# Kernel tuning notes

Hardware: AMD Instinct MI355X
Metric: run time of the kernel (lower is better)

Reference implementation:

```python
import jax, jax.numpy as jnp
import numpy as np
import math

# LLaMA-7B-style int8 attention (torch-int Int8LlamaAttention)
B, S, HID, NH, HD = 2, 1024, 4096, 32, 128
THETA = 10000.0
# per-tensor quantization scales (as produced by from_float)
S_IN, S_W, S_B = 0.02, 0.01, 0.1
S_Q, S_K, S_V, S_O = 0.05, 0.05, 0.05, 0.05


def _rope_tables(position_ids):
    inv_freq = 1.0 / (THETA ** (jnp.arange(0, HD, 2, dtype=jnp.float32) / HD))
    freqs = position_ids.astype(jnp.float32)[..., None] * inv_freq  # [B,S,HD//2]
    emb = jnp.concatenate([freqs, freqs], axis=-1)  # [B,S,HD]
    return jnp.cos(emb)[:, None], jnp.sin(emb)[:, None]  # [B,1,S,HD]


def _rotate_half(x):
    return jnp.concatenate([-x[..., HD // 2:], x[..., :HD // 2]], axis=-1)


def _quant_i8(x):
    return jnp.clip(jnp.round(x), -128, 127).astype(jnp.int8)


def _w8a8b8o8(x_i8, w_i8, b_i8, alpha, beta):
    # int8 GEMM with int32 accumulation, fused dequant-requant to int8
    acc = jnp.einsum('bsk,nk->bsn', x_i8.astype(jnp.int32), w_i8.astype(jnp.int32))
    return _quant_i8(acc.astype(jnp.float32) * alpha + b_i8.astype(jnp.float32) * beta)


def setup_inputs() -> dict:
    key = jax.random.key(0)
    ks = jax.random.split(key, 9)
    ri8 = lambda k, shp: jax.random.randint(k, shp, -127, 128, dtype=jnp.int8)
    return {
        'hidden_states': jax.random.normal(ks[0], (B, S, HID), jnp.float32),
        'position_ids': jnp.broadcast_to(jnp.arange(S, dtype=jnp.int32), (B, S)),
        'w_q': ri8(ks[1], (HID, HID)),
        'w_k': ri8(ks[2], (HID, HID)),
        'w_v': ri8(ks[3], (HID, HID)),
        'w_o': ri8(ks[4], (HID, HID)),
        'b_q': ri8(ks[5], (HID,)),
        'b_k': ri8(ks[6], (HID,)),
        'b_v': ri8(ks[7], (HID,)),
        'b_o': jax.random.normal(ks[8], (HID,), jnp.float32) * 0.01,
    }


def reference(hidden_states, position_ids, w_q, w_k, w_v, w_o, b_q, b_k, b_v, b_o):
    # quantize activations, run int8 q/k/v projections (W8A8B8O8Linear)
    x_i8 = _quant_i8(hidden_states / S_IN)
    q = _w8a8b8o8(x_i8, w_q, b_q, S_IN * S_W / S_Q, S_B / S_Q)
    k = _w8a8b8o8(x_i8, w_k, b_k, S_IN * S_W / S_K, S_B / S_K)
    v = _w8a8b8o8(x_i8, w_v, b_v, S_IN * S_W / S_V, S_B / S_V)
    to_heads = lambda t: t.reshape(B, S, NH, HD).transpose(0, 2, 1, 3)  # [B,NH,S,HD]
    q, k, v = to_heads(q), to_heads(k), to_heads(v)
    # RoPE applied on dequantized int8 values, requantized for the int8 qk bmm
    cos, sin = _rope_tables(position_ids)
    qf, kf = q.astype(jnp.float32), k.astype(jnp.float32)
    q_i8 = _quant_i8(qf * cos + _rotate_half(qf) * sin)
    k_i8 = _quant_i8(kf * cos + _rotate_half(kf) * sin)
    # BMM_S8T_S8N_F32T: int8 QK^T -> fp32 with scale s_q*s_k, then /sqrt(d)
    attn = jnp.einsum('bhsd,bhtd->bhst', q_i8.astype(jnp.int32), k_i8.astype(jnp.int32))
    attn = attn.astype(jnp.float32) * (S_Q * S_K) / math.sqrt(HD)
    # NOTE: source never applies the attention mask (`attn_weights = attn_weights`)
    p = jax.nn.softmax(attn, axis=-1)
    # probs quantized to int8 with scale 1/127 for BMM_S8T_S8N_S8T
    p_i8 = _quant_i8(p * 127.0)
    ctx = jnp.einsum('bhst,bhtd->bhsd', p_i8.astype(jnp.int32), v.astype(jnp.int32))
    ctx_i8 = _quant_i8(ctx.astype(jnp.float32) * ((1.0 / 127.0) * S_V / S_O))
    ctx_i8 = ctx_i8.transpose(0, 2, 1, 3).reshape(B, S, HID)
    # W8A8BFP32OFP32 o_proj: int8 GEMM, fp32 output + fp32 bias
    out = jnp.einsum('bsk,nk->bsn', ctx_i8.astype(jnp.int32), w_o.astype(jnp.int32))
    return out.astype(jnp.float32) * (S_O * S_W) + b_o
```

## Files before the change

### kernel.cpp

```cpp
#include <hip/hip_runtime.h>
#include <hip/hip_bf16.h>
#include <cstdint>
#include <cstddef>

typedef int v4i __attribute__((ext_vector_type(4)));

#define NH 32
#define HD 128
#define SEQ 1024
#define HID 4096
#define BB 2
#define BKB 128

__device__ __forceinline__ signed char quant_i8(float x) {
    float r = rintf(x);
    r = fminf(fmaxf(r, -128.0f), 127.0f);
    return (signed char)r;
}

#define GLOAD_LDS16(g, l) \
    __builtin_amdgcn_global_load_lds((const __attribute__((address_space(1))) void*)(g), \
                                     (__attribute__((address_space(3))) void*)(l), 16, 0, 0)

__global__ __launch_bounds__(256) void pack4_i8_kernel(
    const int* __restrict__ s0, const int* __restrict__ s1,
    const int* __restrict__ s2, const int* __restrict__ s3,
    signed char* __restrict__ d0, signed char* __restrict__ d1,
    signed char* __restrict__ d2, signed char* __restrict__ d3, int n4)
{
    int i = blockIdx.x * 256 + threadIdx.x;
    int which = i / n4;
    int idx = i - which * n4;
    const int* src = (which == 0) ? s0 : (which == 1) ? s1 : (which == 2) ? s2 : s3;
    signed char* dst = (which == 0) ? d0 : (which == 1) ? d1 : (which == 2) ? d2 : d3;
    int4 v = ((const int4*)src)[idx];
    char4 c;
    c.x = (signed char)v.x; c.y = (signed char)v.y;
    c.z = (signed char)v.z; c.w = (signed char)v.w;
    ((char4*)dst)[idx] = c;
}

__global__ __launch_bounds__(256) void quant_x_kernel(const float* __restrict__ src,
                                                      signed char* __restrict__ dst, int n4) {
    int i = blockIdx.x * 256 + threadIdx.x;
    if (i >= n4) return;
    float4 v = ((const float4*)src)[i];
    char4 c;
    c.x = quant_i8(v.x * 50.0f);
    c.y = quant_i8(v.y * 50.0f);
    c.z = quant_i8(v.z * 50.0f);
    c.w = quant_i8(v.w * 50.0f);
    ((char4*)dst)[i] = c;
}

template<bool F32OUT>
__global__ __launch_bounds__(256) void gemm_i8_lds(
    const signed char* __restrict__ A, const signed char* __restrict__ Bw,
    const void* __restrict__ bias, void* __restrict__ outp,
    int M, int N, int K, float alpha, float beta)
{
    __shared__ __align__(16) signed char sA[128 * BKB];
    __shared__ __align__(16) signed char sB[128 * BKB];

    const int t    = threadIdx.x;
    const int w    = t >> 6;
    const int lane = t & 63;
    const int m0   = blockIdx.y * 128;
    const int n0   = blockIdx.x * 128;
    const int lm   = lane & 15;
    const int quad = lane >> 4;
    const int wm   = (w >> 1) * 64;
    const int wn   = (w & 1) * 64;

    int srow[4], skc[4];
    #pragma unroll
    for (int p = 0; p < 4; p++) {
        int si = t + 256 * p;
        int row = si >> 3;
        srow[p] = row;
        skc[p] = ((si & 7) - (row >> 1)) & 7;
    }

    v4i acc[4][4] = {};

    for (int k0 = 0; k0 < K; k0 += BKB) {
        __syncthreads();
        #pragma unroll
        for (int p = 0; p < 4; p++) {
            const signed char* ga = A + (size_t)(m0 + srow[p]) * K + k0 + skc[p] * 16;
            GLOAD_LDS16(ga, sA + t * 16 + p * 4096);
        }
        #pragma unroll
        for (int p = 0; p < 4; p++) {
            const signed char* gb = Bw + (size_t)(n0 + srow[p]) * K + k0 + skc[p] * 16;
            GLOAD_LDS16(gb, sB + t * 16 + p * 4096);
        }
        __syncthreads();

        #pragma unroll
        for (int ks = 0; ks < 2; ks++) {
            v4i af[4], bf[4];
            #pragma unroll
            for (int i = 0; i < 4; i++) {
                int row = wm + 16 * i + lm;
                int slot = (ks * 4 + quad + (lm >> 1)) & 7;
                af[i] = *(const v4i*)(sA + row * BKB + slot * 16);
            }
            #pragma unroll
            for (int j = 0; j < 4; j++) {
                int row = wn + 16 * j + lm;
                int slot = (ks * 4 + quad + (lm >> 1)) & 7;
                bf[j] = *(const v4i*)(sB + row * BKB + slot * 16);
            }
            #pragma unroll
            for (int i = 0; i < 4; i++)
                #pragma unroll
                for (int j = 0; j < 4; j++)
                    acc[i][j] = __builtin_amdgcn_mfma_i32_16x16x64_i8(af[i], bf[j], acc[i][j], 0, 0, 0);
        }
    }

    const int orow = quad * 4;
    #pragma unroll
    for (int i = 0; i < 4; i++) {
        #pragma unroll
        for (int j = 0; j < 4; j++) {
            #pragma unroll
            for (int r = 0; r < 4; r++) {
                int row = m0 + wm + 16 * i + orow + r;
                int col = n0 + wn + 16 * j + lm;
                float v = (float)acc[i][j][r];
                if (F32OUT) {
                    ((float*)outp)[(size_t)row * N + col] = v * alpha + ((const float*)bias)[col];
                } else {
                    float q = v * alpha + (float)((const int*)bias)[col] * beta;
                    ((signed char*)outp)[(size_t)row * N + col] = quant_i8(q);
                }
            }
        }
    }
}

__global__ __launch_bounds__(128) void rope_kernel(
    const int* __restrict__ pos_ids, signed char* __restrict__ q,
    signed char* __restrict__ k, const signed char* __restrict__ v,
    signed char* __restrict__ vt)
{
    int bid = blockIdx.x;
    int h = bid & (NH - 1);
    int s = (bid >> 5) & (SEQ - 1);
    int b = bid >> 15;
    int d = threadIdx.x;
    size_t base = ((size_t)(b * SEQ + s) * NH + h) * (size_t)HD;
    int pos = pos_ids[b * SEQ + s];

    float inv = expf(-(float)(2 * (d & 63)) * (9.210340371976184f / 128.0f));
    float freq = (float)pos * inv;
    float cs = cosf(freq), sn = sinf(freq);

    float qd = (float)q[base + d];
    float qp = (float)q[base + (d ^ 64)];
    float kd = (float)k[base + d];
    float kp = (float)k[base + (d ^ 64)];
    signed char vd = v[base + d];
    __syncthreads();

    float rotq = (d < 64) ? -qp : qp;
    float rotk = (d < 64) ? -kp : kp;
    q[base + d] = quant_i8(qd * cs + rotq * sn);
    k[base + d] = quant_i8(kd * cs + rotk * sn);
    vt[((size_t)((b * NH + h) * HD + d)) * SEQ + s] = vd;
}

__global__ __launch_bounds__(256) void attn_kernel(
    const signed char* __restrict__ q, const signed char* __restrict__ k,
    const signed char* __restrict__ vt, signed char* __restrict__ ctx)
{
    __shared__ __align__(16) char smem[65536];
    float* sc = (float*)smem;
    signed char* p8 = (signed char*)smem;

    const int w    = threadIdx.x >> 6;
    const int lane = threadIdx.x & 63;
    const int bid  = blockIdx.x;
    const int mt   = bid & 63;
    const int bh   = bid >> 6;
    const int b    = bh >> 5, h = bh & 31;
    const int m0   = mt * 16;
    const int lm   = lane & 15;
    const int lkb  = (lane >> 4) * 16;
    const int quad = lane >> 4;

    const float SCALE = 0.0025f / 11.313708498984761f;
    const float LOG2E = 1.4426950408889634f;

    const signed char* qbase = q + ((size_t)(b * SEQ + m0 + lm) * NH + h) * (size_t)HD + lkb;
    v4i a0 = *(const v4i*)qbase;
    v4i a1 = *(const v4i*)(qbase + 64);

    #pragma unroll
    for (int j = 0; j < 16; j++) {
        int col = w * 256 + j * 16;
        const signed char* kb = k + ((size_t)(b * SEQ + col + lm) * NH + h) * (size_t)HD + lkb;
        v4i b0 = *(const v4i*)kb;
        v4i b1 = *(const v4i*)(kb + 64);
        v4i acc = {};
        acc = __builtin_amdgcn_mfma_i32_16x16x64_i8(a0, b0, acc, 0, 0, 0);
        acc = __builtin_amdgcn_mfma_i32_16x16x64_i8(a1, b1, acc, 0, 0, 0);
        #pragma unroll
        for (int r = 0; r < 4; r++) {
            int row = quad * 4 + r;
            sc[row * 1024 + col + lm] = (float)acc[r] * SCALE;
        }
    }
    __syncthreads();

    int packed[4][4];
    #pragma unroll
    for (int r = 0; r < 4; r++) {
        int row = w * 4 + r;
        float vals[16];
        #pragma unroll
        for (int c = 0; c < 4; c++) {
            float4 f = *(const float4*)(sc + row * 1024 + c * 256 + lane * 4);
            vals[c * 4 + 0] = f.x; vals[c * 4 + 1] = f.y;
            vals[c * 4 + 2] = f.z; vals[c * 4 + 3] = f.w;
        }
        float mx = -1e30f;
        #pragma unroll
        for (int t = 0; t < 16; t++) mx = fmaxf(mx, vals[t]);
        #pragma unroll
        for (int off = 32; off >= 1; off >>= 1) mx = fmaxf(mx, __shfl_xor(mx, off));
        float sum = 0.f;
        #pragma unroll
        for (int t = 0; t < 16; t++) { vals[t] = exp2f((vals[t] - mx) * LOG2E); sum += vals[t]; }
        #pragma unroll
        for (int off = 32; off >= 1; off >>= 1) sum += __shfl_xor(sum, off);
        float sf = 127.0f / sum;
        #pragma unroll
        for (int c = 0; c < 4; c++) {
            union { signed char cc[4]; int ii; } u;
            #pragma unroll
            for (int t = 0; t < 4; t++) u.cc[t] = quant_i8(vals[c * 4 + t] * sf);
            packed[r][c] = u.ii;
        }
    }
    __syncthreads();

    #pragma unroll
    for (int r = 0; r < 4; r++)
        #pragma unroll
        for (int c = 0; c < 4; c++)
            *(int*)(p8 + (w * 4 + r) * 1040 + c * 256 + lane * 4) = packed[r][c];
    __syncthreads();

    v4i accp[2] = {};
    for (int kk = 0; kk < SEQ; kk += 64) {
        v4i af = *(const v4i*)(p8 + lm * 1040 + kk + lkb);
        #pragma unroll
        for (int j = 0; j < 2; j++) {
            int col = w * 32 + j * 16;
            const signed char* vb = vt + ((size_t)(bh * HD + col + lm)) * (size_t)SEQ + kk + lkb;
            accp[j] = __builtin_amdgcn_mfma_i32_16x16x64_i8(af, *(const v4i*)vb, accp[j], 0, 0, 0);
        }
    }
    #pragma unroll
    for (int j = 0; j < 2; j++) {
        #pragma unroll
        for (int r = 0; r < 4; r++) {
            int row = quad * 4 + r;
            int col = w * 32 + j * 16 + lm;
            ctx[((size_t)(b * SEQ + m0 + row) * NH + h) * (size_t)HD + col] =
                quant_i8((float)accp[j][r] * (1.0f / 127.0f));
        }
    }
}

extern "C" void kernel_launch(void* const* d_in, const int* in_sizes, int n_in,
                              void* d_out, int out_size, void* d_ws, size_t ws_size,
                              hipStream_t stream)
{
    const float* hidden = (const float*)d_in[0];
    const int* pos_ids  = (const int*)d_in[1];
    const int* w_q = (const int*)d_in[2];
    const int* w_k = (const int*)d_in[3];
    const int* w_v = (const int*)d_in[4];
    const int* w_o = (const int*)d_in[5];
    const int* b_q = (const int*)d_in[6];
    const int* b_k = (const int*)d_in[7];
    const int* b_v = (const int*)d_in[8];
    const float* b_o = (const float*)d_in[9];
    float* out = (float*)d_out;

    char* ws = (char*)d_ws;
    const size_t WSZ = (size_t)HID * HID;
    signed char* wq8 = (signed char*)ws;
    signed char* wk8 = wq8 + WSZ;
    signed char* wv8 = wk8 + WSZ;
    signed char* wo8 = wv8 + WSZ;
    signed char* x8  = wo8 + WSZ;
    const size_t ASZ = (size_t)BB * SEQ * HID;
    signed char* q8  = x8 + ASZ;
    signed char* k8  = q8 + ASZ;
    signed char* v8  = k8 + ASZ;
    signed char* vt8 = v8 + ASZ;
    signed char* c8  = vt8 + ASZ;

    int wn4 = HID * HID / 4;
    pack4_i8_kernel<<<4 * wn4 / 256, 256, 0, stream>>>(w_q, w_k, w_v, w_o,
                                                       wq8, wk8, wv8, wo8, wn4);
    int xn4 = (int)(ASZ / 4);
    quant_x_kernel<<<xn4 / 256, 256, 0, stream>>>(hidden, x8, xn4);

    dim3 g(HID / 128, BB * SEQ / 128);
    gemm_i8_lds<false><<<g, 256, 0, stream>>>(x8, wq8, b_q, q8, BB * SEQ, HID, HID, 0.004f, 2.0f);
    gemm_i8_lds<false><<<g, 256, 0, stream>>>(x8, wk8, b_k, k8, BB * SEQ, HID, HID, 0.004f, 2.0f);
    gemm_i8_lds<false><<<g, 256, 0, stream>>>(x8, wv8, b_v, v8, BB * SEQ, HID, HID, 0.004f, 2.0f);

    rope_kernel<<<BB * SEQ * NH, 128, 0, stream>>>(pos_ids, q8, k8, v8, vt8);
    attn_kernel<<<BB * NH * (SEQ / 16), 256, 0, stream>>>(q8, k8, vt8, c8);

    gemm_i8_lds<true><<<g, 256, 0, stream>>>(c8, wo8, b_o, out, BB * SEQ, HID, HID, 0.0005f, 0.0f);
}
```

Before: 636.4 us.

## Fuse QKV GEMMs, shrink o-proj tile, batch RoPE rows, register-resident softmax

Merges the three Q/K/V projection GEMMs into one launch of 96x16 blocks, so the GPU sees one larger grid and the activation tile is shared through cache. The output projection switches to a 64-row M tile to double the block count. The RoPE kernel now handles 8 sequence positions per block and writes V-transpose with 8-byte stores instead of single-byte scatters. The attention kernel keeps scores in registers with the Q/K MFMA operands swapped, and does the softmax reductions through a small LDS buffer. This cuts the 64KB score buffer and raises occupancy, at the cost of higher register pressure.

```diff
diff --git a/kernel.cpp b/kernel.cpp
--- a/kernel.cpp
+++ b/kernel.cpp
@@ -53,55 +53,63 @@
     ((char4*)dst)[i] = c;
 }
 
-template<bool F32OUT>
-__global__ __launch_bounds__(256) void gemm_i8_lds(
+template<int TM, bool F32OUT>
+__device__ __forceinline__ void gemm_core(
     const signed char* __restrict__ A, const signed char* __restrict__ Bw,
     const void* __restrict__ bias, void* __restrict__ outp,
-    int M, int N, int K, float alpha, float beta)
-{
-    __shared__ __align__(16) signed char sA[128 * BKB];
+    int m0, int n0, int N, int K, float alpha, float beta)
+{
+    constexpr int MI = TM / 32;
+    constexpr int PA = TM / 32;
+    __shared__ __align__(16) signed char sA[TM * BKB];
     __shared__ __align__(16) signed char sB[128 * BKB];
 
     const int t    = threadIdx.x;
     const int w    = t >> 6;
     const int lane = t & 63;
-    const int m0   = blockIdx.y * 128;
-    const int n0   = blockIdx.x * 128;
     const int lm   = lane & 15;
     const int quad = lane >> 4;
-    const int wm   = (w >> 1) * 64;
+    const int wm   = (w >> 1) * (TM / 2);
     const int wn   = (w & 1) * 64;
 
-    int srow[4], skc[4];
+    int srowA[PA], skcA[PA];
+    #pragma unroll
+    for (int p = 0; p < PA; p++) {
+        int si = t + 256 * p;
+        int row = si >> 3;
+        srowA[p] = row;
+        skcA[p] = ((si & 7) - (row >> 1)) & 7;
+    }
+    int srowB[4], skcB[4];
     #pragma unroll
     for (int p = 0; p < 4; p++) {
         int si = t + 256 * p;
         int row = si >> 3;
-        srow[p] = row;
-        skc[p] = ((si & 7) - (row >> 1)) & 7;
-    }
-
-    v4i acc[4][4] = {};
+        srowB[p] = row;
+        skcB[p] = ((si & 7) - (row >> 1)) & 7;
+    }
+
+    v4i acc[MI][4] = {};
 
     for (int k0 = 0; k0 < K; k0 += BKB) {
         __syncthreads();
         #pragma unroll
+        for (int p = 0; p < PA; p++) {
+            const signed char* ga = A + (size_t)(m0 + srowA[p]) * K + k0 + skcA[p] * 16;
+            GLOAD_LDS16(ga, sA + t * 16 + p * 4096);
+        }
+        #pragma unroll
         for (int p = 0; p < 4; p++) {
-            const signed char* ga = A + (size_t)(m0 + srow[p]) * K + k0 + skc[p] * 16;
-            GLOAD_LDS16(ga, sA + t * 16 + p * 4096);
-        }
-        #pragma unroll
-        for (int p = 0; p < 4; p++) {
-            const signed char* gb = Bw + (size_t)(n0 + srow[p]) * K + k0 + skc[p] * 16;
+            const signed char* gb = Bw + (size_t)(n0 + srowB[p]) * K + k0 + skcB[p] * 16;
             GLOAD_LDS16(gb, sB + t * 16 + p * 4096);
         }
         __syncthreads();
 
         #pragma unroll
         for (int ks = 0; ks < 2; ks++) {
-            v4i af[4], bf[4];
+            v4i af[MI], bf[4];
             #pragma unroll
-            for (int i = 0; i < 4; i++) {
+            for (int i = 0; i < MI; i++) {
                 int row = wm + 16 * i + lm;
                 int slot = (ks * 4 + quad + (lm >> 1)) & 7;
                 af[i] = *(const v4i*)(sA + row * BKB + slot * 16);
@@ -113,7 +121,7 @@
                 bf[j] = *(const v4i*)(sB + row * BKB + slot * 16);
             }
             #pragma unroll
-            for (int i = 0; i < 4; i++)
+            for (int i = 0; i < MI; i++)
                 #pragma unroll
                 for (int j = 0; j < 4; j++)
                     acc[i][j] = __builtin_amdgcn_mfma_i32_16x16x64_i8(af[i], bf[j], acc[i][j], 0, 0, 0);
@@ -122,7 +130,7 @@
 
     const int orow = quad * 4;
     #pragma unroll
-    for (int i = 0; i < 4; i++) {
+    for (int i = 0; i < MI; i++) {
         #pragma unroll
         for (int j = 0; j < 4; j++) {
             #pragma unroll
@@ -141,44 +149,83 @@
     }
 }
 
+__global__ __launch_bounds__(256) void gemm_qkv(
+    const signed char* __restrict__ x8,
+    const signed char* __restrict__ wq, const signed char* __restrict__ wk,
+    const signed char* __restrict__ wv,
+    const int* __restrict__ bq, const int* __restrict__ bk, const int* __restrict__ bv,
+    signed char* __restrict__ q8, signed char* __restrict__ k8, signed char* __restrict__ v8)
+{
+    const int nblk = blockIdx.x;
+    const int which = nblk >> 5;
+    const int n0 = (nblk & 31) * 128;
+    const int m0 = blockIdx.y * 128;
+    const signed char* Bw = (which == 0) ? wq : (which == 1) ? wk : wv;
+    const int* bias = (which == 0) ? bq : (which == 1) ? bk : bv;
+    signed char* outp = (which == 0) ? q8 : (which == 1) ? k8 : v8;
+    gemm_core<128, false>(x8, Bw, bias, outp, m0, n0, HID, HID, 0.004f, 2.0f);
+}
+
+__global__ __launch_bounds__(256) void gemm_o(
+    const signed char* __restrict__ c8, const signed char* __restrict__ wo,
+    const float* __restrict__ bo, float* __restrict__ outp)
+{
+    gemm_core<64, true>(c8, wo, bo, outp, blockIdx.y * 64, blockIdx.x * 128,
+                        HID, HID, 0.0005f, 0.0f);
+}
+
 __global__ __launch_bounds__(128) void rope_kernel(
     const int* __restrict__ pos_ids, signed char* __restrict__ q,
     signed char* __restrict__ k, const signed char* __restrict__ v,
     signed char* __restrict__ vt)
 {
-    int bid = blockIdx.x;
-    int h = bid & (NH - 1);
-    int s = (bid >> 5) & (SEQ - 1);
-    int b = bid >> 15;
-    int d = threadIdx.x;
-    size_t base = ((size_t)(b * SEQ + s) * NH + h) * (size_t)HD;
-    int pos = pos_ids[b * SEQ + s];
+    const int bid = blockIdx.x;
+    const int sg = bid & 127;
+    const int h  = (bid >> 7) & (NH - 1);
+    const int b  = bid >> 12;
+    const int d  = threadIdx.x;
+    const int s0 = sg * 8;
+    const int bh = b * NH + h;
 
     float inv = expf(-(float)(2 * (d & 63)) * (9.210340371976184f / 128.0f));
-    float freq = (float)pos * inv;
-    float cs = cosf(freq), sn = sinf(freq);
-
-    float qd = (float)q[base + d];
-    float qp = (float)q[base + (d ^ 64)];
-    float kd = (float)k[base + d];
-    float kp = (float)k[base + (d ^ 64)];
-    signed char vd = v[base + d];
-    __syncthreads();
-
-    float rotq = (d < 64) ? -qp : qp;
-    float rotk = (d < 64) ? -kp : kp;
-    q[base + d] = quant_i8(qd * cs + rotq * sn);
-    k[base + d] = quant_i8(kd * cs + rotk * sn);
-    vt[((size_t)((b * NH + h) * HD + d)) * SEQ + s] = vd;
-}
-
-__global__ __launch_bounds__(256) void attn_kernel(
+
+    float qd[8], qp[8], kd[8], kp[8];
+    signed char vd[8];
+    int pos[8];
+    size_t base[8];
+    #pragma unroll
+    for (int i = 0; i < 8; i++) {
+        int s = s0 + i;
+        base[i] = ((size_t)(b * SEQ + s) * NH + h) * (size_t)HD;
+        pos[i] = pos_ids[b * SEQ + s];
+        qd[i] = (float)q[base[i] + d];
+        qp[i] = (float)q[base[i] + (d ^ 64)];
+        kd[i] = (float)k[base[i] + d];
+        kp[i] = (float)k[base[i] + (d ^ 64)];
+        vd[i] = v[base[i] + d];
+    }
+    __syncthreads();
+
+    union { signed char c[8]; int2 i2; } vu;
+    #pragma unroll
+    for (int i = 0; i < 8; i++) {
+        float freq = (float)pos[i] * inv;
+        float cs = cosf(freq), sn = sinf(freq);
+        float rotq = (d < 64) ? -qp[i] : qp[i];
+        float rotk = (d < 64) ? -kp[i] : kp[i];
+        q[base[i] + d] = quant_i8(qd[i] * cs + rotq * sn);
+        k[base[i] + d] = quant_i8(kd[i] * cs + rotk * sn);
+        vu.c[i] = vd[i];
+    }
+    *(int2*)(vt + ((size_t)(bh * HD + d)) * SEQ + s0) = vu.i2;
+}
+
+__global__ __launch_bounds__(256, 4) void attn_kernel(
     const signed char* __restrict__ q, const signed char* __restrict__ k,
     const signed char* __restrict__ vt, signed char* __restrict__ ctx)
 {
-    __shared__ __align__(16) char smem[65536];
-    float* sc = (float*)smem;
-    signed char* p8 = (signed char*)smem;
+    __shared__ __align__(16) signed char p8[16 * 1040];
+    __shared__ float red[64];
 
     const int w    = threadIdx.x >> 6;
     const int lane = threadIdx.x & 63;
@@ -188,72 +235,66 @@
     const int b    = bh >> 5, h = bh & 31;
     const int m0   = mt * 16;
     const int lm   = lane & 15;
-    const int lkb  = (lane >> 4) * 16;
     const int quad = lane >> 4;
 
     const float SCALE = 0.0025f / 11.313708498984761f;
     const float LOG2E = 1.4426950408889634f;
 
-    const signed char* qbase = q + ((size_t)(b * SEQ + m0 + lm) * NH + h) * (size_t)HD + lkb;
-    v4i a0 = *(const v4i*)qbase;
-    v4i a1 = *(const v4i*)(qbase + 64);
-
+    const signed char* qbase = q + ((size_t)(b * SEQ + m0 + lm) * NH + h) * (size_t)HD + quad * 16;
+    v4i qb0 = *(const v4i*)qbase;
+    v4i qb1 = *(const v4i*)(qbase + 64);
+
+    float vals[16][4];
     #pragma unroll
     for (int j = 0; j < 16; j++) {
-        int col = w * 256 + j * 16;
-        const signed char* kb = k + ((size_t)(b * SEQ + col + lm) * NH + h) * (size_t)HD + lkb;
-        v4i b0 = *(const v4i*)kb;
-        v4i b1 = *(const v4i*)(kb + 64);
+        int t0 = w * 256 + j * 16;
+        const signed char* kb = k + ((size_t)(b * SEQ + t0 + lm) * NH + h) * (size_t)HD + quad * 16;
+        v4i a0 = *(const v4i*)kb;
+        v4i a1 = *(const v4i*)(kb + 64);
         v4i acc = {};
-        acc = __builtin_amdgcn_mfma_i32_16x16x64_i8(a0, b0, acc, 0, 0, 0);
-        acc = __builtin_amdgcn_mfma_i32_16x16x64_i8(a1, b1, acc, 0, 0, 0);
+        acc = __builtin_amdgcn_mfma_i32_16x16x64_i8(a0, qb0, acc, 0, 0, 0);
+        acc = __builtin_amdgcn_mfma_i32_16x16x64_i8(a1, qb1, acc, 0, 0, 0);
+        #pragma unroll
+        for (int r = 0; r < 4; r++) vals[j][r] = (float)acc[r] * SCALE;
+    }
+
+    float mx = vals[0][0];
+    #pragma unroll
+    for (int j = 0; j < 16; j++)
+        #pragma unroll
+        for (int r = 0; r < 4; r++) mx = fmaxf(mx, vals[j][r]);
+    mx = fmaxf(mx, __shfl_xor(mx, 16));
+    mx = fmaxf(mx, __shfl_xor(mx, 32));
+    if (lane < 16) red[w * 16 + lane] = mx;
+    __syncthreads();
+    mx = fmaxf(fmaxf(red[lm], red[16 + lm]), fmaxf(red[32 + lm], red[48 + lm]));
+
+    float sum = 0.f;
+    #pragma unroll
+    for (int j = 0; j < 16; j++)
         #pragma unroll
         for (int r = 0; r < 4; r++) {
-            int row = quad * 4 + r;
-            sc[row * 1024 + col + lm] = (float)acc[r] * SCALE;
-        }
-    }
-    __syncthreads();
-
-    int packed[4][4];
-    #pragma unroll
-    for (int r = 0; r < 4; r++) {
-        int row = w * 4 + r;
-        float vals[16];
-        #pragma unroll
-        for (int c = 0; c < 4; c++) {
-            float4 f = *(const float4*)(sc + row * 1024 + c * 256 + lane * 4);
-            vals[c * 4 + 0] = f.x; vals[c * 4 + 1] = f.y;
-            vals[c * 4 + 2] = f.z; vals[c * 4 + 3] = f.w;
-        }
-        float mx = -1e30f;
-        #pragma unroll
-        for (int t = 0; t < 16; t++) mx = fmaxf(mx, vals[t]);
-        #pragma unroll
-        for (int off = 32; off >= 1; off >>= 1) mx = fmaxf(mx, __shfl_xor(mx, off));
-        float sum = 0.f;
-        #pragma unroll
-        for (int t = 0; t < 16; t++) { vals[t] = exp2f((vals[t] - mx) * LOG2E); sum += vals[t]; }
-        #pragma unroll
-        for (int off = 32; off >= 1; off >>= 1) sum += __shfl_xor(sum, off);
-        float sf = 127.0f / sum;
-        #pragma unroll
-        for (int c = 0; c < 4; c++) {
-            union { signed char cc[4]; int ii; } u;
-            #pragma unroll
-            for (int t = 0; t < 4; t++) u.cc[t] = quant_i8(vals[c * 4 + t] * sf);
-            packed[r][c] = u.ii;
-        }
-    }
-    __syncthreads();
-
-    #pragma unroll
-    for (int r = 0; r < 4; r++)
-        #pragma unroll
-        for (int c = 0; c < 4; c++)
-            *(int*)(p8 + (w * 4 + r) * 1040 + c * 256 + lane * 4) = packed[r][c];
-    __syncthreads();
-
+            vals[j][r] = exp2f((vals[j][r] - mx) * LOG2E);
+            sum += vals[j][r];
+        }
+    sum += __shfl_xor(sum, 16);
+    sum += __shfl_xor(sum, 32);
+    __syncthreads();
+    if (lane < 16) red[w * 16 + lane] = sum;
+    __syncthreads();
+    sum = (red[lm] + red[16 + lm]) + (red[32 + lm] + red[48 + lm]);
+    float sf = 127.0f / sum;
+
+    #pragma unroll
+    for (int j = 0; j < 16; j++) {
+        union { signed char cc[4]; int ii; } u;
+        #pragma unroll
+        for (int r = 0; r < 4; r++) u.cc[r] = quant_i8(vals[j][r] * sf);
+        *(int*)(p8 + lm * 1040 + w * 256 + j * 16 + quad * 4) = u.ii;
+    }
+    __syncthreads();
+
+    const int lkb = quad * 16;
     v4i accp[2] = {};
     for (int kk = 0; kk < SEQ; kk += 64) {
         v4i af = *(const v4i*)(p8 + lm * 1040 + kk + lkb);
@@ -312,13 +353,11 @@
     int xn4 = (int)(ASZ / 4);
     quant_x_kernel<<<xn4 / 256, 256, 0, stream>>>(hidden, x8, xn4);
 
-    dim3 g(HID / 128, BB * SEQ / 128);
-    gemm_i8_lds<false><<<g, 256, 0, stream>>>(x8, wq8, b_q, q8, BB * SEQ, HID, HID, 0.004f, 2.0f);
-    gemm_i8_lds<false><<<g, 256, 0, stream>>>(x8, wk8, b_k, k8, BB * SEQ, HID, HID, 0.004f, 2.0f);
-    gemm_i8_lds<false><<<g, 256, 0, stream>>>(x8, wv8, b_v, v8, BB * SEQ, HID, HID, 0.004f, 2.0f);
-
-    rope_kernel<<<BB * SEQ * NH, 128, 0, stream>>>(pos_ids, q8, k8, v8, vt8);
+    gemm_qkv<<<dim3(96, 16), 256, 0, stream>>>(x8, wq8, wk8, wv8, b_q, b_k, b_v,
+                                               q8, k8, v8);
+
+    rope_kernel<<<BB * NH * (SEQ / 8), 128, 0, stream>>>(pos_ids, q8, k8, v8, vt8);
     attn_kernel<<<BB * NH * (SEQ / 16), 256, 0, stream>>>(q8, k8, vt8, c8);
 
-    gemm_i8_lds<true><<<g, 256, 0, stream>>>(c8, wo8, b_o, out, BB * SEQ, HID, HID, 0.0005f, 0.0f);
-}
+    gemm_o<<<dim3(32, 32), 256, 0, stream>>>(c8, wo8, b_o, out);
+}
```

Result: faster. 604.8 us (-5.0%).
